# Kernel tuning notes

Measured on AMD Instinct MI355X. Metric: run time of the kernel, lower is better.

Reference implementation:

```python
import jax, jax.numpy as jnp
import numpy as np

N, E, H, L, G = 50000, 500000, 128, 4, 1000
EPS = 1e-7      # GENConv message eps
LN_EPS = 1e-5   # torch LayerNorm default


def setup_inputs() -> dict:
    key = jax.random.key(0)
    ks = jax.random.split(key, 24)
    d = {}
    d["x"] = jax.random.normal(ks[0], (N, 9), jnp.float32)
    d["edge_index"] = jax.random.randint(ks[1], (2, E), 0, N, jnp.int32)
    d["edge_attr"] = jax.random.normal(ks[2], (E, 3), jnp.float32)
    d["batch"] = jnp.sort(jax.random.randint(ks[3], (N,), 0, G, jnp.int32))
    s9, s3, sh, s2h = 1/np.sqrt(9), 1/np.sqrt(3), 1/np.sqrt(H), 1/np.sqrt(2*H)
    u = lambda k, shp, s: jax.random.uniform(k, shp, jnp.float32, -s, s)
    d["enc_node_W"] = u(ks[4], (9, H), s9)
    d["enc_node_b"] = u(ks[5], (H,), s9)
    d["enc_edge_W"] = u(ks[6], (3, H), s3)
    d["enc_edge_b"] = u(ks[7], (H,), s3)
    d["ln_g"] = jnp.ones((L, H), jnp.float32)   # DeepGCNLayer pre-norm affine
    d["ln_b"] = jnp.zeros((L, H), jnp.float32)
    d["W1"] = u(ks[8], (L, H, 2*H), sh)          # GENConv MLP layer 1
    d["b1"] = u(ks[9], (L, 2*H), sh)
    d["mlp_ln_g"] = jnp.ones((L, 2*H), jnp.float32)
    d["mlp_ln_b"] = jnp.zeros((L, 2*H), jnp.float32)
    d["W2"] = u(ks[10], (L, 2*H, H), s2h)        # GENConv MLP layer 2
    d["b2"] = u(ks[11], (L, H), s2h)
    d["t"] = jnp.ones((L,), jnp.float32)         # learnable softmax temperature, init 1.0
    return d


def layernorm(x, g, b):
    mu = x.mean(-1, keepdims=True)
    var = ((x - mu) ** 2).mean(-1, keepdims=True)
    return (x - mu) / jnp.sqrt(var + LN_EPS) * g + b


def genconv(h, src, dst, ea, t, W1, b1, lg, lb, W2, b2):
    # message: relu(x_j + edge_attr) + eps   -> [E, H]
    msg = jax.nn.relu(h[src] + ea) + EPS
    # softmax aggregation over incoming edges, per channel
    logits = t * msg
    m = jax.ops.segment_max(logits, dst, num_segments=N)
    num = jnp.exp(logits - m[dst])
    den = jax.ops.segment_sum(num, dst, num_segments=N)
    alpha = num / den[dst]
    agg = jax.ops.segment_sum(msg * alpha, dst, num_segments=N)
    out = agg + h  # root residual inside GENConv
    z = jax.nn.relu(layernorm(out @ W1 + b1, lg, lb))
    return z @ W2 + b2


def reference(x, edge_index, edge_attr, batch, enc_node_W, enc_node_b,
              enc_edge_W, enc_edge_b, ln_g, ln_b, W1, b1, mlp_ln_g, mlp_ln_b,
              W2, b2, t):
    src, dst = edge_index[0], edge_index[1]
    h = x @ enc_node_W + enc_node_b            # node encoder  [N, H]
    ea = edge_attr @ enc_edge_W + enc_edge_b   # edge encoder  [E, H]
    # layer 0: conv only (DeeperGCN forward uses layers[0].conv directly)
    h = genconv(h, src, dst, ea, t[0], W1[0], b1[0], mlp_ln_g[0], mlp_ln_b[0], W2[0], b2[0])
    # layers 1..L-1: res+ block: x + conv(relu(LN(x))); dropout is identity (eval)
    for i in range(1, L):
        z = jax.nn.relu(layernorm(h, ln_g[i], ln_b[i]))
        h = h + genconv(z, src, dst, ea, t[i], W1[i], b1[i], mlp_ln_g[i], mlp_ln_b[i], W2[i], b2[i])
    h = jax.nn.relu(layernorm(h, ln_g[0], ln_b[0]))  # reuses layer-0 norm
    # global mean pool over graphs
    counts = jax.ops.segment_sum(jnp.ones((N,), h.dtype), batch, num_segments=G)
    sums = jax.ops.segment_sum(h, batch, num_segments=G)
    return sums / jnp.maximum(counts, 1.0)[:, None]
```

## Files before the change

kernel.cpp:

```cpp
#include <hip/hip_runtime.h>

#define NN 50000
#define NE 500000
#define HD 128
#define HD2 256
#define NL 4
#define NG 1000

constexpr float MSG_EPS = 1e-7f;
constexpr float LNEPS   = 1e-5f;

typedef float  f32x4  __attribute__((ext_vector_type(4)));
typedef __bf16 bf16x8 __attribute__((ext_vector_type(8)));

__device__ __forceinline__ unsigned short f2b(float f) {
    unsigned int u = __float_as_uint(f);
    unsigned int r = u + 0x7FFFu + ((u >> 16) & 1u);
    return (unsigned short)(r >> 16);
}
__device__ __forceinline__ float b2f(unsigned short h) {
    return __uint_as_float(((unsigned int)h) << 16);
}

__global__ void k_encode_nodes(const float* __restrict__ x, const float* __restrict__ W,
                               const float* __restrict__ b, unsigned short* __restrict__ zb) {
    int n = blockIdx.x;
    int c = threadIdx.x;
    float xr[9];
#pragma unroll
    for (int k = 0; k < 9; k++) xr[k] = x[n * 9 + k];
    float acc = b[c];
#pragma unroll
    for (int k = 0; k < 9; k++) acc = fmaf(xr[k], W[k * HD + c], acc);
    zb[n * HD + c] = f2b(acc);
}

__global__ void k_prep(const float* __restrict__ W1, const float* __restrict__ W2,
                       unsigned short* __restrict__ W1T, unsigned short* __restrict__ W2T) {
    int idx = blockIdx.x * 256 + threadIdx.x;
    {
        int k = idx & 127, n = (idx >> 7) & 255, l = idx >> 15;
        W1T[idx] = f2b(W1[(l * 128 + k) * 256 + n]);
    }
    {
        int k = idx & 255, n = (idx >> 8) & 127, l = idx >> 15;
        W2T[idx] = f2b(W2[(l * 256 + k) * 128 + n]);
    }
}

__global__ void k_hist(const int* __restrict__ dst, int* __restrict__ counts) {
    int e = blockIdx.x * blockDim.x + threadIdx.x;
    if (e < NE) atomicAdd(&counts[dst[e]], 1);
}

#define SCAN_B 512
__global__ void k_scan1(const int* __restrict__ counts, int* __restrict__ incl,
                        int* __restrict__ bsum) {
    __shared__ int s[SCAN_B];
    int i = blockIdx.x * SCAN_B + threadIdx.x;
    int v = (i < NN) ? counts[i] : 0;
    s[threadIdx.x] = v;
    __syncthreads();
    for (int off = 1; off < SCAN_B; off <<= 1) {
        int t = (threadIdx.x >= off) ? s[threadIdx.x - off] : 0;
        __syncthreads();
        s[threadIdx.x] += t;
        __syncthreads();
    }
    if (i < NN) incl[i] = s[threadIdx.x];
    if (threadIdx.x == SCAN_B - 1) bsum[blockIdx.x] = s[threadIdx.x];
}

__global__ void k_scan2(const int* __restrict__ bsum, int* __restrict__ boff, int nb) {
    __shared__ int s[128];
    int v = (threadIdx.x < nb) ? bsum[threadIdx.x] : 0;
    s[threadIdx.x] = v;
    __syncthreads();
    for (int off = 1; off < 128; off <<= 1) {
        int t = (threadIdx.x >= off) ? s[threadIdx.x - off] : 0;
        __syncthreads();
        s[threadIdx.x] += t;
        __syncthreads();
    }
    if (threadIdx.x < nb) boff[threadIdx.x] = s[threadIdx.x] - v;
}

__global__ void k_scan3(const int* __restrict__ incl, const int* __restrict__ boff,
                        int* __restrict__ row_start) {
    int i = blockIdx.x * SCAN_B + threadIdx.x;
    if (i < NN) row_start[i + 1] = incl[i] + boff[blockIdx.x];
    if (i == 0) row_start[0] = 0;
}

__global__ void k_scatter(const int* __restrict__ src, const int* __restrict__ dst,
                          const float* __restrict__ eattr, const int* __restrict__ row_start,
                          int* __restrict__ cursor, float4* __restrict__ aperm) {
    int e = blockIdx.x * blockDim.x + threadIdx.x;
    if (e >= NE) return;
    int d = dst[e];
    int p = row_start[d] + atomicAdd(&cursor[d], 1);
    float4 v;
    v.x = eattr[e * 3 + 0];
    v.y = eattr[e * 3 + 1];
    v.z = eattr[e * 3 + 2];
    v.w = __int_as_float(src[e]);
    aperm[p] = v;
}

__device__ __forceinline__ void edge_acc1(float4 a, float z, float w0, float w1, float w2,
                                          float bb, float tv, float& num, float& wm) {
    float ea = fmaf(a.x, w0, fmaf(a.y, w1, fmaf(a.z, w2, bb)));
    float m = fmaxf(z + ea, 0.f) + MSG_EPS;
    float e = __expf(tv * m);
    num += e;
    wm = fmaf(m, e, wm);
}

__global__ __launch_bounds__(256) void k_aggregate(const unsigned short* __restrict__ zbin,
                                                   const float4* __restrict__ aperm,
                                                   const int* __restrict__ row_start,
                                                   const float* __restrict__ We,
                                                   const float* __restrict__ be,
                                                   const float* __restrict__ t, int layer,
                                                   unsigned short* __restrict__ outb) {
    int w = threadIdx.x >> 6, lane = threadIdx.x & 63;
    int n = blockIdx.x * 2 + (w >> 1);
    if (n >= NN) return;
    int c = ((w & 1) << 6) | lane;
    float w0 = We[c], w1 = We[HD + c], w2 = We[2 * HD + c], bb = be[c];
    float tv = t[layer];
    int s0 = row_start[n], s1 = row_start[n + 1];
    float num = 0.f, wm = 0.f;
    int p = s0;
    for (; p + 4 <= s1; p += 4) {
        float4 a0 = aperm[p], a1 = aperm[p + 1], a2 = aperm[p + 2], a3 = aperm[p + 3];
        float z0 = b2f(zbin[(size_t)__float_as_int(a0.w) * HD + c]);
        float z1 = b2f(zbin[(size_t)__float_as_int(a1.w) * HD + c]);
        float z2 = b2f(zbin[(size_t)__float_as_int(a2.w) * HD + c]);
        float z3 = b2f(zbin[(size_t)__float_as_int(a3.w) * HD + c]);
        edge_acc1(a0, z0, w0, w1, w2, bb, tv, num, wm);
        edge_acc1(a1, z1, w0, w1, w2, bb, tv, num, wm);
        edge_acc1(a2, z2, w0, w1, w2, bb, tv, num, wm);
        edge_acc1(a3, z3, w0, w1, w2, bb, tv, num, wm);
    }
    for (; p < s1; p++) {
        float4 a = aperm[p];
        float z = b2f(zbin[(size_t)__float_as_int(a.w) * HD + c]);
        edge_acc1(a, z, w0, w1, w2, bb, tv, num, wm);
    }
    float zn = b2f(zbin[(size_t)n * HD + c]);
    float o = ((s1 > s0) ? (wm / num) : 0.f) + zn;
    outb[(size_t)n * HD + c] = f2b(o);
}

#define BM 32
#define HS_LD 264

__global__ __launch_bounds__(256) void k_mlp(const unsigned short* __restrict__ outb,
                                             const unsigned short* __restrict__ W1T,
                                             const float* __restrict__ b1l,
                                             const float* __restrict__ lgl,
                                             const float* __restrict__ lbl,
                                             const unsigned short* __restrict__ W2T,
                                             const float* __restrict__ b2l,
                                             unsigned short* __restrict__ h,
                                             const float* __restrict__ gn,
                                             const float* __restrict__ bn,
                                             unsigned short* __restrict__ zb,
                                             int add_residual) {
    __shared__ __align__(16) unsigned short Hs[BM * HS_LD];
    __shared__ __align__(16) float2 st1[2][16][4];
    __shared__ __align__(16) float2 st2[2][16][4];

    int nb = blockIdx.x * BM;
    int tid = threadIdx.x;
    int w = tid >> 6, lane = tid & 63, q = lane >> 4, i = lane & 15;

    f32x4 acc[2][4];
#pragma unroll
    for (int rt = 0; rt < 2; rt++)
#pragma unroll
        for (int ct = 0; ct < 4; ct++) acc[rt][ct] = (f32x4){0.f, 0.f, 0.f, 0.f};

    bf16x8 acur[2], bcur[4];
#pragma unroll
    for (int rt = 0; rt < 2; rt++) {
        int row = nb + rt * 16 + i;
        acur[rt] = (row < NN) ? *(const bf16x8*)&outb[(size_t)row * HD + q * 8]
                              : (bf16x8)(__bf16)0.f;
    }
#pragma unroll
    for (int ct = 0; ct < 4; ct++)
        bcur[ct] = *(const bf16x8*)&W1T[(w * 64 + ct * 16 + i) * HD + q * 8];

#pragma unroll
    for (int ks = 0; ks < 4; ks++) {
        bf16x8 anxt[2], bnxt[4];
        if (ks < 3) {
#pragma unroll
            for (int rt = 0; rt < 2; rt++) {
                int row = nb + rt * 16 + i;
                anxt[rt] = (row < NN)
                               ? *(const bf16x8*)&outb[(size_t)row * HD + (ks + 1) * 32 + q * 8]
                               : (bf16x8)(__bf16)0.f;
            }
#pragma unroll
            for (int ct = 0; ct < 4; ct++)
                bnxt[ct] =
                    *(const bf16x8*)&W1T[(w * 64 + ct * 16 + i) * HD + (ks + 1) * 32 + q * 8];
        }
#pragma unroll
        for (int rt = 0; rt < 2; rt++)
#pragma unroll
            for (int ct = 0; ct < 4; ct++)
                acc[rt][ct] =
                    __builtin_amdgcn_mfma_f32_16x16x32_bf16(acur[rt], bcur[ct], acc[rt][ct],
                                                            0, 0, 0);
        if (ks < 3) {
#pragma unroll
            for (int rt = 0; rt < 2; rt++) acur[rt] = anxt[rt];
#pragma unroll
            for (int ct = 0; ct < 4; ct++) bcur[ct] = bnxt[ct];
        }
    }

#pragma unroll
    for (int ct = 0; ct < 4; ct++) {
        float bb = b1l[w * 64 + ct * 16 + i];
#pragma unroll
        for (int rt = 0; rt < 2; rt++)
#pragma unroll
            for (int r = 0; r < 4; r++) acc[rt][ct][r] += bb;
    }

    {
        float sv[2][4], qv[2][4];
#pragma unroll
        for (int rt = 0; rt < 2; rt++)
#pragma unroll
            for (int r = 0; r < 4; r++) {
                float s = acc[rt][0][r] + acc[rt][1][r] + acc[rt][2][r] + acc[rt][3][r];
                float sq = 0.f;
#pragma unroll
                for (int ct = 0; ct < 4; ct++) sq = fmaf(acc[rt][ct][r], acc[rt][ct][r], sq);
                sv[rt][r] = s;
                qv[rt][r] = sq;
            }
#pragma unroll
        for (int m = 1; m <= 8; m <<= 1)
#pragma unroll
            for (int rt = 0; rt < 2; rt++)
#pragma unroll
                for (int r = 0; r < 4; r++) {
                    sv[rt][r] += __shfl_xor(sv[rt][r], m);
                    qv[rt][r] += __shfl_xor(qv[rt][r], m);
                }
        if (i == 0) {
#pragma unroll
            for (int rt = 0; rt < 2; rt++)
#pragma unroll
                for (int r = 0; r < 4; r++)
                    st1[rt][q * 4 + r][w] = make_float2(sv[rt][r], qv[rt][r]);
        }
    }
    __syncthreads();

    {
        float mu[2][4], inv[2][4];
#pragma unroll
        for (int rt = 0; rt < 2; rt++)
#pragma unroll
            for (int r = 0; r < 4; r++) {
                const float4* sp = (const float4*)&st1[rt][q * 4 + r][0];
                float4 a = sp[0], b = sp[1];
                float S = a.x + a.z + b.x + b.z;
                float Q = a.y + a.w + b.y + b.w;
                float m_ = S * (1.f / 256.f);
                float v_ = Q * (1.f / 256.f) - m_ * m_;
                mu[rt][r] = m_;
                inv[rt][r] = rsqrtf(v_ + LNEPS);
            }
#pragma unroll
        for (int ct = 0; ct < 4; ct++) {
            float g = lgl[w * 64 + ct * 16 + i];
            float c = lbl[w * 64 + ct * 16 + i];
#pragma unroll
            for (int rt = 0; rt < 2; rt++)
#pragma unroll
                for (int r = 0; r < 4; r++) {
                    float v =
                        fmaxf(fmaf((acc[rt][ct][r] - mu[rt][r]) * inv[rt][r], g, c), 0.f);
                    Hs[(rt * 16 + q * 4 + r) * HS_LD + w * 64 + ct * 16 + i] = f2b(v);
                }
        }
    }
    __syncthreads();

    unsigned short hold[2][2][4] = {};
    if (add_residual) {
#pragma unroll
        for (int rt = 0; rt < 2; rt++)
#pragma unroll
            for (int ct = 0; ct < 2; ct++)
#pragma unroll
                for (int r = 0; r < 4; r++) {
                    int row = nb + rt * 16 + q * 4 + r;
                    hold[rt][ct][r] =
                        (row < NN) ? h[(size_t)row * HD + w * 32 + ct * 16 + i] : 0;
                }
    }

    f32x4 acc2[2][2];
#pragma unroll
    for (int rt = 0; rt < 2; rt++)
#pragma unroll
        for (int ct = 0; ct < 2; ct++) acc2[rt][ct] = (f32x4){0.f, 0.f, 0.f, 0.f};

    bf16x8 hc[2], bc[2];
#pragma unroll
    for (int rt = 0; rt < 2; rt++) hc[rt] = *(const bf16x8*)&Hs[(rt * 16 + i) * HS_LD + q * 8];
#pragma unroll
    for (int ct = 0; ct < 2; ct++)
        bc[ct] = *(const bf16x8*)&W2T[(w * 32 + ct * 16 + i) * HD2 + q * 8];

#pragma unroll
    for (int ks = 0; ks < 8; ks++) {
        bf16x8 hn[2], bn2[2];
        if (ks < 7) {
#pragma unroll
            for (int rt = 0; rt < 2; rt++)
                hn[rt] = *(const bf16x8*)&Hs[(rt * 16 + i) * HS_LD + (ks + 1) * 32 + q * 8];
#pragma unroll
            for (int ct = 0; ct < 2; ct++)
                bn2[ct] =
                    *(const bf16x8*)&W2T[(w * 32 + ct * 16 + i) * HD2 + (ks + 1) * 32 + q * 8];
        }
#pragma unroll
        for (int rt = 0; rt < 2; rt++)
#pragma unroll
            for (int ct = 0; ct < 2; ct++)
                acc2[rt][ct] = __builtin_amdgcn_mfma_f32_16x16x32_bf16(hc[rt], bc[ct],
                                                                      acc2[rt][ct], 0, 0, 0);
        if (ks < 7) {
#pragma unroll
            for (int rt = 0; rt < 2; rt++) hc[rt] = hn[rt];
#pragma unroll
            for (int ct = 0; ct < 2; ct++) bc[ct] = bn2[ct];
        }
    }

#pragma unroll
    for (int ct = 0; ct < 2; ct++) {
        float bb = b2l[w * 32 + ct * 16 + i];
#pragma unroll
        for (int rt = 0; rt < 2; rt++)
#pragma unroll
            for (int r = 0; r < 4; r++) {
                float v = acc2[rt][ct][r] + bb;
                if (add_residual) v += b2f(hold[rt][ct][r]);
                acc2[rt][ct][r] = v;
                int row = nb + rt * 16 + q * 4 + r;
                if (row < NN) h[(size_t)row * HD + w * 32 + ct * 16 + i] = f2b(v);
            }
    }

    {
        float sv[2][4], qv[2][4];
#pragma unroll
        for (int rt = 0; rt < 2; rt++)
#pragma unroll
            for (int r = 0; r < 4; r++) {
                sv[rt][r] = acc2[rt][0][r] + acc2[rt][1][r];
                qv[rt][r] = fmaf(acc2[rt][0][r], acc2[rt][0][r],
                                 acc2[rt][1][r] * acc2[rt][1][r]);
            }
#pragma unroll
        for (int m = 1; m <= 8; m <<= 1)
#pragma unroll
            for (int rt = 0; rt < 2; rt++)
#pragma unroll
                for (int r = 0; r < 4; r++) {
                    sv[rt][r] += __shfl_xor(sv[rt][r], m);
                    qv[rt][r] += __shfl_xor(qv[rt][r], m);
                }
        if (i == 0) {
#pragma unroll
            for (int rt = 0; rt < 2; rt++)
#pragma unroll
                for (int r = 0; r < 4; r++)
                    st2[rt][q * 4 + r][w] = make_float2(sv[rt][r], qv[rt][r]);
        }
    }
    __syncthreads();

    {
#pragma unroll
        for (int rt = 0; rt < 2; rt++)
#pragma unroll
            for (int r = 0; r < 4; r++) {
                const float4* sp = (const float4*)&st2[rt][q * 4 + r][0];
                float4 a = sp[0], b = sp[1];
                float S = a.x + a.z + b.x + b.z;
                float Q = a.y + a.w + b.y + b.w;
                float m_ = S * (1.f / 128.f);
                float v_ = Q * (1.f / 128.f) - m_ * m_;
                float iv = rsqrtf(v_ + LNEPS);
#pragma unroll
                for (int ct = 0; ct < 2; ct++) {
                    float g = gn[w * 32 + ct * 16 + i];
                    float c = bn[w * 32 + ct * 16 + i];
                    float v = fmaxf(fmaf((acc2[rt][ct][r] - m_) * iv, g, c), 0.f);
                    int row = nb + rt * 16 + q * 4 + r;
                    if (row < NN) zb[(size_t)row * HD + w * 32 + ct * 16 + i] = f2b(v);
                }
            }
    }
}

__global__ void k_gbounds(const int* __restrict__ batch, int* __restrict__ gstart) {
    int g = blockIdx.x * blockDim.x + threadIdx.x;
    if (g > NG) return;
    int lo = 0, hi = NN;
    while (lo < hi) {
        int mid = (lo + hi) >> 1;
        if (batch[mid] < g) lo = mid + 1;
        else hi = mid;
    }
    gstart[g] = lo;
}

__global__ void k_pool(const unsigned short* __restrict__ zb, const int* __restrict__ gstart,
                       float* __restrict__ out) {
    int g = blockIdx.x;
    int c = threadIdx.x;
    int a = gstart[g], b = gstart[g + 1];
    float s0 = 0.f, s1 = 0.f;
    int n = a;
    for (; n + 2 <= b; n += 2) {
        s0 += b2f(zb[(size_t)n * HD + c]);
        s1 += b2f(zb[(size_t)(n + 1) * HD + c]);
    }
    if (n < b) s0 += b2f(zb[(size_t)n * HD + c]);
    out[g * HD + c] = (s0 + s1) / fmaxf((float)(b - a), 1.f);
}

extern "C" void kernel_launch(void* const* d_in, const int* in_sizes, int n_in, void* d_out,
                              int out_size, void* d_ws, size_t ws_size, hipStream_t stream) {
    const float* x     = (const float*)d_in[0];
    const int* ei      = (const int*)d_in[1];
    const float* eattr = (const float*)d_in[2];
    const int* batch   = (const int*)d_in[3];
    const float* encW  = (const float*)d_in[4];
    const float* encB  = (const float*)d_in[5];
    const float* eW    = (const float*)d_in[6];
    const float* eB    = (const float*)d_in[7];
    const float* ln_g  = (const float*)d_in[8];
    const float* ln_b  = (const float*)d_in[9];
    const float* W1    = (const float*)d_in[10];
    const float* b1    = (const float*)d_in[11];
    const float* mlg   = (const float*)d_in[12];
    const float* mlb   = (const float*)d_in[13];
    const float* W2    = (const float*)d_in[14];
    const float* b2    = (const float*)d_in[15];
    const float* t     = (const float*)d_in[16];
    const int* src = ei;
    const int* dst = ei + NE;

    char* w = (char*)d_ws;
    auto alloc = [&](size_t bytes) {
        char* p = w;
        w += (bytes + 255) & ~size_t(255);
        return p;
    };
    unsigned short* h    = (unsigned short*)alloc(sizeof(unsigned short) * NN * HD);
    unsigned short* zb   = (unsigned short*)alloc(sizeof(unsigned short) * NN * HD);
    unsigned short* outb = (unsigned short*)alloc(sizeof(unsigned short) * NN * HD);
    float4* aperm        = (float4*)alloc(sizeof(float4) * NE);
    int* row_start       = (int*)alloc(sizeof(int) * (NN + 1));
    int* counts          = (int*)alloc(sizeof(int) * NN);
    int* cursor          = (int*)alloc(sizeof(int) * NN);
    int* incl            = (int*)alloc(sizeof(int) * NN);
    int* bsum            = (int*)alloc(sizeof(int) * 128);
    int* boff            = (int*)alloc(sizeof(int) * 128);
    int* gstart          = (int*)alloc(sizeof(int) * (NG + 1));
    unsigned short* W1T  = (unsigned short*)alloc(sizeof(unsigned short) * NL * HD * HD2);
    unsigned short* W2T  = (unsigned short*)alloc(sizeof(unsigned short) * NL * HD2 * HD);

    hipMemsetAsync(counts, 0, sizeof(int) * NN, stream);
    hipMemsetAsync(cursor, 0, sizeof(int) * NN, stream);

    k_prep<<<512, 256, 0, stream>>>(W1, W2, W1T, W2T);
    k_encode_nodes<<<NN, HD, 0, stream>>>(x, encW, encB, zb);
    k_hist<<<(NE + 255) / 256, 256, 0, stream>>>(dst, counts);
    int nsb = (NN + SCAN_B - 1) / SCAN_B;
    k_scan1<<<nsb, SCAN_B, 0, stream>>>(counts, incl, bsum);
    k_scan2<<<1, 128, 0, stream>>>(bsum, boff, nsb);
    k_scan3<<<nsb, SCAN_B, 0, stream>>>(incl, boff, row_start);
    k_scatter<<<(NE + 255) / 256, 256, 0, stream>>>(src, dst, eattr, row_start, cursor, aperm);
    k_gbounds<<<(NG + 256) / 256, 256, 0, stream>>>(batch, gstart);

    for (int l = 0; l < NL; l++) {
        k_aggregate<<<(NN + 1) / 2, 256, 0, stream>>>(zb, aperm, row_start, eW, eB, t, l, outb);
        int ln_next = (l + 1) % NL;
        k_mlp<<<(NN + BM - 1) / BM, 256, 0, stream>>>(
            outb, W1T + (size_t)l * HD * HD2, b1 + l * HD2, mlg + l * HD2, mlb + l * HD2,
            W2T + (size_t)l * HD2 * HD, b2 + l * HD, h, ln_g + ln_next * HD,
            ln_b + ln_next * HD, zb, l > 0);
    }
    k_pool<<<NG, HD, 0, stream>>>(zb, gstart, (float*)d_out);
}
```

Baseline: 596.3 us.

## Process one node per wave with packed bf16 pairs; restage MLP epilogue through LDS

The aggregation kernel now assigns one wavefront per destination node, with each lane handling two channels through 32-bit packed bf16 loads. This halves the number of edge-record loads per node and widens the gathers. The MLP epilogue writes the second GEMM's output (plus bias) to a shared tile. A row-per-wave pass then adds the residual, stores h and computes the next layer's LayerNorm with full-wave shuffles instead of cross-wave LDS stats. This costs an extra LDS buffer and sync, and the residual sum is now rounded to bf16 before it is added.

```diff
diff --git a/kernel.cpp b/kernel.cpp
--- a/kernel.cpp
+++ b/kernel.cpp
@@ -20,6 +20,9 @@
 }
 __device__ __forceinline__ float b2f(unsigned short h) {
     return __uint_as_float(((unsigned int)h) << 16);
+}
+__device__ __forceinline__ unsigned int pack2(float a, float b) {
+    return (unsigned int)f2b(a) | ((unsigned int)f2b(b) << 16);
 }
 
 __global__ void k_encode_nodes(const float* __restrict__ x, const float* __restrict__ W,
@@ -107,13 +110,19 @@
     aperm[p] = v;
 }
 
-__device__ __forceinline__ void edge_acc1(float4 a, float z, float w0, float w1, float w2,
-                                          float bb, float tv, float& num, float& wm) {
-    float ea = fmaf(a.x, w0, fmaf(a.y, w1, fmaf(a.z, w2, bb)));
-    float m = fmaxf(z + ea, 0.f) + MSG_EPS;
-    float e = __expf(tv * m);
-    num += e;
-    wm = fmaf(m, e, wm);
+__device__ __forceinline__ void edge_acc2(float4 a, unsigned int zz, float2 w0, float2 w1,
+                                          float2 w2, float2 bb, float tv, float& num0,
+                                          float& num1, float& wm0, float& wm1) {
+    float zx = b2f((unsigned short)zz), zy = b2f((unsigned short)(zz >> 16));
+    float eax = fmaf(a.x, w0.x, fmaf(a.y, w1.x, fmaf(a.z, w2.x, bb.x)));
+    float eay = fmaf(a.x, w0.y, fmaf(a.y, w1.y, fmaf(a.z, w2.y, bb.y)));
+    float mx = fmaxf(zx + eax, 0.f) + MSG_EPS;
+    float my = fmaxf(zy + eay, 0.f) + MSG_EPS;
+    float ex = __expf(tv * mx), ey = __expf(tv * my);
+    num0 += ex;
+    num1 += ey;
+    wm0 = fmaf(mx, ex, wm0);
+    wm1 = fmaf(my, ey, wm1);
 }
 
 __global__ __launch_bounds__(256) void k_aggregate(const unsigned short* __restrict__ zbin,
@@ -122,39 +131,45 @@
                                                    const float* __restrict__ We,
                                                    const float* __restrict__ be,
                                                    const float* __restrict__ t, int layer,
-                                                   unsigned short* __restrict__ outb) {
+                                                   unsigned int* __restrict__ outb) {
     int w = threadIdx.x >> 6, lane = threadIdx.x & 63;
-    int n = blockIdx.x * 2 + (w >> 1);
+    int n = blockIdx.x * 4 + w;
     if (n >= NN) return;
-    int c = ((w & 1) << 6) | lane;
-    float w0 = We[c], w1 = We[HD + c], w2 = We[2 * HD + c], bb = be[c];
+    int c = lane * 2;
+    float2 w0 = *(const float2*)&We[c];
+    float2 w1 = *(const float2*)&We[HD + c];
+    float2 w2 = *(const float2*)&We[2 * HD + c];
+    float2 bb = *(const float2*)&be[c];
     float tv = t[layer];
     int s0 = row_start[n], s1 = row_start[n + 1];
-    float num = 0.f, wm = 0.f;
+    float num0 = 0.f, num1 = 0.f, wm0 = 0.f, wm1 = 0.f;
+    const unsigned int* z32 = (const unsigned int*)zbin;
     int p = s0;
     for (; p + 4 <= s1; p += 4) {
         float4 a0 = aperm[p], a1 = aperm[p + 1], a2 = aperm[p + 2], a3 = aperm[p + 3];
-        float z0 = b2f(zbin[(size_t)__float_as_int(a0.w) * HD + c]);
-        float z1 = b2f(zbin[(size_t)__float_as_int(a1.w) * HD + c]);
-        float z2 = b2f(zbin[(size_t)__float_as_int(a2.w) * HD + c]);
-        float z3 = b2f(zbin[(size_t)__float_as_int(a3.w) * HD + c]);
-        edge_acc1(a0, z0, w0, w1, w2, bb, tv, num, wm);
-        edge_acc1(a1, z1, w0, w1, w2, bb, tv, num, wm);
-        edge_acc1(a2, z2, w0, w1, w2, bb, tv, num, wm);
-        edge_acc1(a3, z3, w0, w1, w2, bb, tv, num, wm);
+        unsigned int zz0 = z32[(size_t)__float_as_int(a0.w) * 64 + lane];
+        unsigned int zz1 = z32[(size_t)__float_as_int(a1.w) * 64 + lane];
+        unsigned int zz2 = z32[(size_t)__float_as_int(a2.w) * 64 + lane];
+        unsigned int zz3 = z32[(size_t)__float_as_int(a3.w) * 64 + lane];
+        edge_acc2(a0, zz0, w0, w1, w2, bb, tv, num0, num1, wm0, wm1);
+        edge_acc2(a1, zz1, w0, w1, w2, bb, tv, num0, num1, wm0, wm1);
+        edge_acc2(a2, zz2, w0, w1, w2, bb, tv, num0, num1, wm0, wm1);
+        edge_acc2(a3, zz3, w0, w1, w2, bb, tv, num0, num1, wm0, wm1);
     }
     for (; p < s1; p++) {
         float4 a = aperm[p];
-        float z = b2f(zbin[(size_t)__float_as_int(a.w) * HD + c]);
-        edge_acc1(a, z, w0, w1, w2, bb, tv, num, wm);
-    }
-    float zn = b2f(zbin[(size_t)n * HD + c]);
-    float o = ((s1 > s0) ? (wm / num) : 0.f) + zn;
-    outb[(size_t)n * HD + c] = f2b(o);
+        unsigned int zz = z32[(size_t)__float_as_int(a.w) * 64 + lane];
+        edge_acc2(a, zz, w0, w1, w2, bb, tv, num0, num1, wm0, wm1);
+    }
+    unsigned int zn = z32[(size_t)n * 64 + lane];
+    float ox = ((s1 > s0) ? (wm0 / num0) : 0.f) + b2f((unsigned short)zn);
+    float oy = ((s1 > s0) ? (wm1 / num1) : 0.f) + b2f((unsigned short)(zn >> 16));
+    outb[(size_t)n * 64 + lane] = pack2(ox, oy);
 }
 
 #define BM 32
 #define HS_LD 264
+#define HT_LD 136
 
 __global__ __launch_bounds__(256) void k_mlp(const unsigned short* __restrict__ outb,
                                              const unsigned short* __restrict__ W1T,
@@ -169,8 +184,8 @@
                                              unsigned short* __restrict__ zb,
                                              int add_residual) {
     __shared__ __align__(16) unsigned short Hs[BM * HS_LD];
+    __shared__ __align__(16) unsigned short Ht[BM * HT_LD];
     __shared__ __align__(16) float2 st1[2][16][4];
-    __shared__ __align__(16) float2 st2[2][16][4];
 
     int nb = blockIdx.x * BM;
     int tid = threadIdx.x;
@@ -296,20 +311,6 @@
     }
     __syncthreads();
 
-    unsigned short hold[2][2][4] = {};
-    if (add_residual) {
-#pragma unroll
-        for (int rt = 0; rt < 2; rt++)
-#pragma unroll
-            for (int ct = 0; ct < 2; ct++)
-#pragma unroll
-                for (int r = 0; r < 4; r++) {
-                    int row = nb + rt * 16 + q * 4 + r;
-                    hold[rt][ct][r] =
-                        (row < NN) ? h[(size_t)row * HD + w * 32 + ct * 16 + i] : 0;
-                }
-    }
-
     f32x4 acc2[2][2];
 #pragma unroll
     for (int rt = 0; rt < 2; rt++)
@@ -355,65 +356,42 @@
 #pragma unroll
         for (int rt = 0; rt < 2; rt++)
 #pragma unroll
-            for (int r = 0; r < 4; r++) {
-                float v = acc2[rt][ct][r] + bb;
-                if (add_residual) v += b2f(hold[rt][ct][r]);
-                acc2[rt][ct][r] = v;
-                int row = nb + rt * 16 + q * 4 + r;
-                if (row < NN) h[(size_t)row * HD + w * 32 + ct * 16 + i] = f2b(v);
+            for (int r = 0; r < 4; r++)
+                Ht[(rt * 16 + q * 4 + r) * HT_LD + w * 32 + ct * 16 + i] =
+                    f2b(acc2[rt][ct][r] + bb);
+    }
+    __syncthreads();
+
+    {
+        const unsigned int* Ht32 = (const unsigned int*)Ht;
+        unsigned int* h32 = (unsigned int*)h;
+        unsigned int* zb32 = (unsigned int*)zb;
+        float2 gg = *(const float2*)&gn[lane * 2];
+        float2 cc = *(const float2*)&bn[lane * 2];
+        for (int rr = w; rr < BM; rr += 4) {
+            int row = nb + rr;
+            if (row >= NN) break;
+            unsigned int tv = Ht32[rr * (HT_LD / 2) + lane];
+            float cx = b2f((unsigned short)tv), cy = b2f((unsigned short)(tv >> 16));
+            if (add_residual) {
+                unsigned int hv = h32[(size_t)row * 64 + lane];
+                cx += b2f((unsigned short)hv);
+                cy += b2f((unsigned short)(hv >> 16));
             }
-    }
-
-    {
-        float sv[2][4], qv[2][4];
-#pragma unroll
-        for (int rt = 0; rt < 2; rt++)
-#pragma unroll
-            for (int r = 0; r < 4; r++) {
-                sv[rt][r] = acc2[rt][0][r] + acc2[rt][1][r];
-                qv[rt][r] = fmaf(acc2[rt][0][r], acc2[rt][0][r],
-                                 acc2[rt][1][r] * acc2[rt][1][r]);
+            h32[(size_t)row * 64 + lane] = pack2(cx, cy);
+            float s = cx + cy, sq = cx * cx + cy * cy;
+#pragma unroll
+            for (int m = 32; m >= 1; m >>= 1) {
+                s += __shfl_xor(s, m);
+                sq += __shfl_xor(sq, m);
             }
-#pragma unroll
-        for (int m = 1; m <= 8; m <<= 1)
-#pragma unroll
-            for (int rt = 0; rt < 2; rt++)
-#pragma unroll
-                for (int r = 0; r < 4; r++) {
-                    sv[rt][r] += __shfl_xor(sv[rt][r], m);
-                    qv[rt][r] += __shfl_xor(qv[rt][r], m);
-                }
-        if (i == 0) {
-#pragma unroll
-            for (int rt = 0; rt < 2; rt++)
-#pragma unroll
-                for (int r = 0; r < 4; r++)
-                    st2[rt][q * 4 + r][w] = make_float2(sv[rt][r], qv[rt][r]);
-        }
-    }
-    __syncthreads();
-
-    {
-#pragma unroll
-        for (int rt = 0; rt < 2; rt++)
-#pragma unroll
-            for (int r = 0; r < 4; r++) {
-                const float4* sp = (const float4*)&st2[rt][q * 4 + r][0];
-                float4 a = sp[0], b = sp[1];
-                float S = a.x + a.z + b.x + b.z;
-                float Q = a.y + a.w + b.y + b.w;
-                float m_ = S * (1.f / 128.f);
-                float v_ = Q * (1.f / 128.f) - m_ * m_;
-                float iv = rsqrtf(v_ + LNEPS);
-#pragma unroll
-                for (int ct = 0; ct < 2; ct++) {
-                    float g = gn[w * 32 + ct * 16 + i];
-                    float c = bn[w * 32 + ct * 16 + i];
-                    float v = fmaxf(fmaf((acc2[rt][ct][r] - m_) * iv, g, c), 0.f);
-                    int row = nb + rt * 16 + q * 4 + r;
-                    if (row < NN) zb[(size_t)row * HD + w * 32 + ct * 16 + i] = f2b(v);
-                }
-            }
+            float mu = s * (1.f / 128.f);
+            float var = sq * (1.f / 128.f) - mu * mu;
+            float inv = rsqrtf(var + LNEPS);
+            float z0 = fmaxf(fmaf((cx - mu) * inv, gg.x, cc.x), 0.f);
+            float z1 = fmaxf(fmaf((cy - mu) * inv, gg.y, cc.y), 0.f);
+            zb32[(size_t)row * 64 + lane] = pack2(z0, z1);
+        }
     }
 }
 
@@ -474,7 +452,7 @@
     };
     unsigned short* h    = (unsigned short*)alloc(sizeof(unsigned short) * NN * HD);
     unsigned short* zb   = (unsigned short*)alloc(sizeof(unsigned short) * NN * HD);
-    unsigned short* outb = (unsigned short*)alloc(sizeof(unsigned short) * NN * HD);
+    unsigned int* outb   = (unsigned int*)alloc(sizeof(unsigned int) * NN * HD / 2);
     float4* aperm        = (float4*)alloc(sizeof(float4) * NE);
     int* row_start       = (int*)alloc(sizeof(int) * (NN + 1));
     int* counts          = (int*)alloc(sizeof(int) * NN);
@@ -500,12 +478,12 @@
     k_gbounds<<<(NG + 256) / 256, 256, 0, stream>>>(batch, gstart);
 
     for (int l = 0; l < NL; l++) {
-        k_aggregate<<<(NN + 1) / 2, 256, 0, stream>>>(zb, aperm, row_start, eW, eB, t, l, outb);
+        k_aggregate<<<(NN + 3) / 4, 256, 0, stream>>>(zb, aperm, row_start, eW, eB, t, l, outb);
         int ln_next = (l + 1) % NL;
         k_mlp<<<(NN + BM - 1) / BM, 256, 0, stream>>>(
-            outb, W1T + (size_t)l * HD * HD2, b1 + l * HD2, mlg + l * HD2, mlb + l * HD2,
-            W2T + (size_t)l * HD2 * HD, b2 + l * HD, h, ln_g + ln_next * HD,
-            ln_b + ln_next * HD, zb, l > 0);
+            (const unsigned short*)outb, W1T + (size_t)l * HD * HD2, b1 + l * HD2,
+            mlg + l * HD2, mlb + l * HD2, W2T + (size_t)l * HD2 * HD, b2 + l * HD, h,
+            ln_g + ln_next * HD, ln_b + ln_next * HD, zb, l > 0);
     }
     k_pool<<<NG, HD, 0, stream>>>(zb, gstart, (float*)d_out);
 }
```

Measured after the change: 506.1 us. -15.1%, faster.
